# Kernel tuning notes

Hardware: AMD Instinct MI355X
Metric: run time of the kernel (lower is better)

Reference implementation:

```python
import jax, jax.numpy as jnp
import numpy as np

B = 32       # batch
IN_N = 32    # input capsules
IN_D = 16    # input capsule dim (== out_d)
H = 14       # input spatial
OUT_N = 32   # output capsules
OUT_D = 16
HO = 7       # parent grid h_out = w_out
HID = 64     # Linformer projection dim
EPS = 1e-5


def _gconv(x, w, groups):
    # x: [b, C, H, W], w: [C_out, C_in/groups, kh, kw]; stride 1, pad 1
    return jax.lax.conv_general_dilated(
        x, w, window_strides=(1, 1), padding=((1, 1), (1, 1)),
        dimension_numbers=("NCHW", "OIHW", "NCHW"), feature_group_count=groups)


def setup_inputs() -> dict:
    key = jax.random.key(0)
    ks = jax.random.split(key, 7)
    current_pose = jax.random.normal(ks[0], (B, IN_N, H, H, IN_D), dtype=jnp.float32)
    next_pose = jax.random.normal(ks[1], (B, OUT_N, HO, HO, OUT_D), dtype=jnp.float32)
    # grouped conv weights (torch layout OIHW, groups = IN_N)
    current_w = 0.05 * jax.random.normal(ks[2], (IN_N * IN_D, IN_D, 3, 3), dtype=jnp.float32)
    next_w = 0.05 * jax.random.normal(ks[3], (OUT_N * OUT_D, OUT_N * OUT_D // IN_N, 3, 3), dtype=jnp.float32)
    E_proj = 0.02 * jax.random.normal(ks[4], (IN_N, H * H, HID), dtype=jnp.float32)
    rel_embedd = jax.random.normal(ks[5], (IN_D, HO * HO), dtype=jnp.float32)
    ln_gamma = jnp.ones((OUT_D,), dtype=jnp.float32)
    ln_beta = jnp.zeros((OUT_D,), dtype=jnp.float32)
    return {
        "current_pose": current_pose, "next_pose": next_pose,
        "current_w": current_w, "next_w": next_w,
        "E_proj": E_proj, "rel_embedd": rel_embedd,
        "ln_gamma": ln_gamma, "ln_beta": ln_beta,
        "num_iter": 1,
    }


def reference(current_pose, next_pose, current_w, next_w, E_proj, rel_embedd,
              ln_gamma, ln_beta, num_iter):
    b = current_pose.shape[0]
    # 5D -> [b, n*d, H, W]
    cp = current_pose.transpose(0, 2, 3, 1, 4).reshape(b, H, H, IN_N * IN_D)
    cp = cp.transpose(0, 3, 1, 2)
    cp = _gconv(cp, current_w, IN_N)                       # [b, n*d, H, H]
    # headwise Linformer key projection
    cp = cp.reshape(b, IN_D, IN_N, 1, H * H)
    k = jnp.matmul(cp, E_proj)                             # [b, d, n, 1, HID]
    k = k.reshape(b, IN_D, IN_N * HID).transpose(0, 2, 1)  # [b, n*HID, d]
    rel = jnp.broadcast_to(rel_embedd.T[None], (b, HO * HO, IN_D))
    k = jnp.concatenate([k, rel], axis=1)                  # [b, N, d]

    # parent pose -> queries
    q = next_pose.transpose(0, 2, 3, 1, 4).reshape(b, HO, HO, OUT_N * OUT_D)
    q = q.transpose(0, 3, 1, 2)
    q = _gconv(q, next_w, IN_N)                            # [b, out_n*out_d, HO, HO]
    q = q.reshape(b, OUT_N * HO * HO, OUT_D)               # [b, J, d]

    dots = jnp.einsum("bje,bie->bji", q, k) * (IN_D ** -0.5)  # [b, J, N]
    dots = jax.nn.softmax(dots, axis=-2)                   # softmax over queries j
    out = jnp.einsum("bji,bie->bje", dots, k)              # [b, J, d]

    out = out.reshape(b, OUT_N * IN_D, HO, HO)
    out = _gconv(out, next_w, IN_N)
    out = out.reshape(b, OUT_N, HO, HO, IN_D)

    # LayerNorm over last dim (dropout rate = 0)
    mu = out.mean(-1, keepdims=True)
    var = ((out - mu) ** 2).mean(-1, keepdims=True)
    out = (out - mu) / jnp.sqrt(var + EPS) * ln_gamma + ln_beta
    return out
```

## Files before the change

kernel.cpp:

```cpp
#include <hip/hip_runtime.h>

typedef unsigned short u16;
typedef __attribute__((ext_vector_type(8))) short short8;
typedef __attribute__((ext_vector_type(4))) float floatx4;

#define MFMA16(a, b, c) __builtin_amdgcn_mfma_f32_16x16x32_bf16(a, b, c, 0, 0, 0)

__device__ inline u16 bf16rn(float x) {
    unsigned u = __float_as_uint(x);
    u += 0x7fffu + ((u >> 16) & 1u);
    return (u16)(u >> 16);
}
__device__ inline float bf16tof(u16 h) { return __uint_as_float(((unsigned)h) << 16); }
__device__ inline short8 ld8(const u16* p) { return *(const short8*)p; }

__global__ __launch_bounds__(256) void k_ecvt2(const float* __restrict__ E,
                                               const float* __restrict__ rel,
                                               const float* __restrict__ w,
                                               u16* __restrict__ EhT,
                                               u16* __restrict__ ElT,
                                               u16* __restrict__ Kh,
                                               u16* __restrict__ Kl,
                                               u16* __restrict__ KhT,
                                               u16* __restrict__ KlT,
                                               float* __restrict__ w2) {
    int blk = blockIdx.x, tid = threadIdx.x;
    if (blk < 32) {
        __shared__ float ep[196 * 65];
        int m = blk;
        const float* eb = E + (size_t)m * 12544;
        for (int t = tid; t < 12544; t += 256) {
            int p = t >> 6, h = t & 63;
            ep[p * 65 + h] = eb[t];
        }
        __syncthreads();
        for (int t = tid; t < 64 * 224; t += 256) {
            int h = t / 224, p = t % 224;
            float v = (p < 196) ? ep[p * 65 + h] : 0.f;
            u16 hi = bf16rn(v);
            u16 lo = bf16rn(v - bf16tof(hi));
            EhT[(size_t)m * 14336 + t] = hi;
            ElT[(size_t)m * 14336 + t] = lo;
        }
    } else if (blk < 64) {
        int b = blk - 32;
        size_t bK = (size_t)b * 2112;
        size_t bT = (size_t)b * 33792;
#pragma unroll
        for (int k = 0; k < 4; ++k) {
            int idx = tid + k * 256;
            int row = idx >> 4, e = idx & 15;
            int i = 2048 + row;
            float v = (row < 49) ? rel[e * 49 + row] : 0.f;
            u16 h = bf16rn(v);
            u16 l = bf16rn(v - bf16tof(h));
            Kh[(bK + i) * 16 + e] = h;
            Kl[(bK + i) * 16 + e] = l;
            KhT[bT + (size_t)e * 2112 + i] = h;
            KlT[bT + (size_t)e * 2112 + i] = l;
        }
    } else {
        int g0 = (blk - 64) * 4;
        for (int t = tid; t < 4 * 2304; t += 256) {
            int g = g0 + t / 2304, r = t % 2304;
            int oc = r / 144, rr = r % 144;
            w2[(size_t)g * 2304 + (rr / 9) * 144 + oc * 9 + (rr % 9)] =
                w[(size_t)g * 2304 + r];
        }
    }
}

__global__ __launch_bounds__(256) void k_conv14(const float* __restrict__ pose,
                                                const float* __restrict__ w2,
                                                float* __restrict__ out) {
    int blk = blockIdx.x;
    int oh = blk & 1, bg = blk >> 1;
    int tid = threadIdx.x;
    __shared__ float patch[16 * 256];
#pragma unroll
    for (int k = 0; k < 16; ++k) patch[k * 256 + tid] = 0.f;
    __syncthreads();
    const float* pin = pose + (size_t)bg * 3136;
    for (int t = tid; t < 3136; t += 256) {
        int p = t >> 4, ic = t & 15;
        int y = p / 14, x = p % 14;
        patch[ic * 256 + (y + 1) * 16 + (x + 1)] = pin[t];
    }
    __syncthreads();
    int g = bg & 31;
    const float* wg = w2 + (size_t)g * 2304 + oh * 72;
    float* po = out + (size_t)bg * 3136 + oh * 8 * 196;
    if (tid < 196) {
        int y = tid / 14, x = tid % 14;
        int base = (y + 1) * 16 + (x + 1);
        float acc[8];
#pragma unroll
        for (int oc = 0; oc < 8; ++oc) acc[oc] = 0.f;
        for (int ic = 0; ic < 16; ++ic) {
            const float* pr = patch + ic * 256 + base;
            float win[9];
#pragma unroll
            for (int ky = 0; ky < 3; ++ky)
#pragma unroll
                for (int kx = 0; kx < 3; ++kx)
                    win[ky * 3 + kx] = pr[(ky - 1) * 16 + (kx - 1)];
            const float* wi = wg + ic * 144;
#pragma unroll
            for (int oc = 0; oc < 8; ++oc)
#pragma unroll
                for (int kk = 0; kk < 9; ++kk)
                    acc[oc] += win[kk] * wi[oc * 9 + kk];
        }
#pragma unroll
        for (int oc = 0; oc < 8; ++oc) po[oc * 196 + tid] = acc[oc];
    }
}

__global__ __launch_bounds__(64) void k_conv7(const float* __restrict__ in,
                                              const float* __restrict__ in2,
                                              const float* __restrict__ w,
                                              float* __restrict__ out, int mode) {
    int blk = blockIdx.x;
    int oh = blk & 1, bg = blk >> 1;
    int tid = threadIdx.x;
    __shared__ float patch[16 * 144];
    for (int t = tid; t < 16 * 144; t += 64) patch[t] = 0.f;
    __syncthreads();
    const float* pin = in + (size_t)bg * 784;
    if (mode == 1) {
        for (int t = tid; t < 784; t += 64) {
            int p = t >> 4, ic = t & 15;
            int y = p / 7, x = p % 7;
            patch[ic * 144 + (y + 1) * 16 + (x + 1)] = pin[t];
        }
    } else {
        const float* pin2 = in2 + (size_t)bg * 784;
        for (int t = tid; t < 784; t += 64) {
            int ic = t / 49, p = t % 49;
            int y = p / 7, x = p % 7;
            patch[ic * 144 + (y + 1) * 16 + (x + 1)] = pin[t] + pin2[t];
        }
    }
    __syncthreads();
    int g = bg & 31;
    const float* wg = w + (size_t)g * 2304 + (size_t)oh * 8 * 144;
    float* po = out + (size_t)bg * 784 + (size_t)oh * 8 * 49;
    if (tid < 49) {
        int y = tid / 7, x = tid % 7;
        int base = (y + 1) * 16 + (x + 1);
        float acc[8];
#pragma unroll
        for (int oc = 0; oc < 8; ++oc) acc[oc] = 0.f;
        for (int ic = 0; ic < 16; ++ic) {
            const float* pr = patch + ic * 144 + base;
            float win[9];
#pragma unroll
            for (int ky = 0; ky < 3; ++ky)
#pragma unroll
                for (int kx = 0; kx < 3; ++kx)
                    win[ky * 3 + kx] = pr[(ky - 1) * 16 + (kx - 1)];
            const float* wi = wg + ic * 9;
#pragma unroll
            for (int oc = 0; oc < 8; ++oc)
#pragma unroll
                for (int kk = 0; kk < 9; ++kk)
                    acc[oc] += win[kk] * wi[oc * 144 + kk];
        }
#pragma unroll
        for (int oc = 0; oc < 8; ++oc) po[oc * 49 + tid] = acc[oc];
    }
}

__global__ __launch_bounds__(256) void k_kproj2(const float* __restrict__ cpconv,
                                                const u16* __restrict__ EhT,
                                                const u16* __restrict__ ElT,
                                                u16* __restrict__ Kh,
                                                u16* __restrict__ Kl,
                                                u16* __restrict__ KhT,
                                                u16* __restrict__ KlT) {
    int blk = blockIdx.x;
    int b = blk >> 5, m = blk & 31;
    int wave = threadIdx.x >> 6, lane = threadIdx.x & 63;
    int ht = wave;
    int n = lane & 15, quad = lane >> 4;

    const float* arow = cpconv + ((size_t)b * 512 + (size_t)n * 32 + m) * 196;
    const u16* bhrow = EhT + ((size_t)m * 64 + ht * 16 + n) * 224;
    const u16* blrow = ElT + ((size_t)m * 64 + ht * 16 + n) * 224;

    floatx4 c = {0.f, 0.f, 0.f, 0.f};
#pragma unroll
    for (int pc = 0; pc < 7; ++pc) {
        int p0 = pc * 32 + quad * 8;
        float av[8];
        if (p0 <= 188) {
            float4 x = *(const float4*)(arow + p0);
            float4 y = *(const float4*)(arow + p0 + 4);
            av[0]=x.x; av[1]=x.y; av[2]=x.z; av[3]=x.w;
            av[4]=y.x; av[5]=y.y; av[6]=y.z; av[7]=y.w;
        } else {
#pragma unroll
            for (int k2 = 0; k2 < 8; ++k2) av[k2] = (p0 + k2 < 196) ? arow[p0 + k2] : 0.f;
        }
        short8 ah, al;
#pragma unroll
        for (int k2 = 0; k2 < 8; ++k2) {
            u16 h = bf16rn(av[k2]);
            ah[k2] = (short)h;
            al[k2] = (short)bf16rn(av[k2] - bf16tof(h));
        }
        short8 bh = ld8(bhrow + pc * 32 + quad * 8);
        short8 bl = ld8(blrow + pc * 32 + quad * 8);
        c = MFMA16(ah, bh, c);
        c = MFMA16(ah, bl, c);
        c = MFMA16(al, bh, c);
    }
    int i = m * 64 + ht * 16 + n;
    size_t bK = (size_t)b * 2112;
    size_t bT = (size_t)b * 33792;
    u16 h[4], l[4];
#pragma unroll
    for (int r = 0; r < 4; ++r) {
        h[r] = bf16rn(c[r]);
        l[r] = bf16rn(c[r] - bf16tof(h[r]));
    }
    *(uint2*)(Kh + (bK + i) * 16 + quad * 4) =
        make_uint2((unsigned)h[0] | ((unsigned)h[1] << 16), (unsigned)h[2] | ((unsigned)h[3] << 16));
    *(uint2*)(Kl + (bK + i) * 16 + quad * 4) =
        make_uint2((unsigned)l[0] | ((unsigned)l[1] << 16), (unsigned)l[2] | ((unsigned)l[3] << 16));
#pragma unroll
    for (int r = 0; r < 4; ++r) {
        KhT[bT + (size_t)(quad * 4 + r) * 2112 + i] = h[r];
        KlT[bT + (size_t)(quad * 4 + r) * 2112 + i] = l[r];
    }
}

__global__ __launch_bounds__(256) void k_cvt(const float* __restrict__ qconv,
                                             u16* __restrict__ Qp) {
    int gid = blockIdx.x * 256 + threadIdx.x;
    const float4* q4 = (const float4*)(qconv + (size_t)gid * 16);
    float4 t0 = q4[0], t1 = q4[1], t2 = q4[2], t3 = q4[3];
    float v[16] = {t0.x,t0.y,t0.z,t0.w, t1.x,t1.y,t1.z,t1.w,
                   t2.x,t2.y,t2.z,t2.w, t3.x,t3.y,t3.z,t3.w};
    unsigned hw[8], lw[8];
#pragma unroll
    for (int t = 0; t < 8; ++t) {
        float x0 = v[2*t] * 0.25f, x1 = v[2*t+1] * 0.25f;
        u16 h0 = bf16rn(x0), h1 = bf16rn(x1);
        u16 l0 = bf16rn(x0 - bf16tof(h0)), l1 = bf16rn(x1 - bf16tof(h1));
        hw[t] = (unsigned)h0 | ((unsigned)h1 << 16);
        lw[t] = (unsigned)l0 | ((unsigned)l1 << 16);
    }
    uint4* r4 = (uint4*)(Qp + (size_t)gid * 32);
    r4[0] = make_uint4(hw[0], hw[1], hw[2], hw[3]);
    r4[1] = make_uint4(hw[4], hw[5], hw[6], hw[7]);
    r4[2] = make_uint4(lw[0], lw[1], lw[2], lw[3]);
    r4[3] = make_uint4(lw[4], lw[5], lw[6], lw[7]);
}

__global__ __launch_bounds__(256) void k_stats4(const u16* __restrict__ Qp,
                                                const u16* __restrict__ Kh,
                                                const u16* __restrict__ Kl,
                                                float* __restrict__ dpart) {
    int blk = blockIdx.x;
    int b = blk / 34; int rem = blk % 34; int jh = rem / 17; int tb = rem % 17;
    int wave = threadIdx.x >> 6, lane = threadIdx.x & 63;
    int it2 = tb * 4 + wave;
    if (it2 >= 66) return;
    int ibase = it2 * 32;
    int n = lane & 15, quad = lane >> 4;
    size_t bK = (size_t)b * 2112;
    const u16* kb = Kh + (bK + ibase + n) * 16 + (quad & 1) * 8;
    const u16* lb = Kl + (bK + ibase + n) * 16 + (quad & 1) * 8;
    short8 bh0 = ld8(kb), bh1 = ld8(kb + 256);
    short8 bl0 = ld8(lb), bl1 = ld8(lb + 256);
    const u16* qb = Qp + (size_t)b * 50176 + (size_t)jh * 49 * 512 + n * 32 + quad * 8;
    floatx4 d0 = {0.f,0.f,0.f,0.f}, d1 = {0.f,0.f,0.f,0.f};
    short8 a0 = ld8(qb), a1 = ld8(qb + 512);
    for (int c = 0; c < 49; ++c) {
        short8 a2 = (c + 2 < 49) ? ld8(qb + (size_t)(c + 2) * 512) : a0;
        floatx4 s0 = {0.f,0.f,0.f,0.f}, s1 = {0.f,0.f,0.f,0.f};
        s0 = MFMA16(a0, bh0, s0);
        s0 = MFMA16(a0, bl0, s0);
        s1 = MFMA16(a0, bh1, s1);
        s1 = MFMA16(a0, bl1, s1);
        d0.x += __expf(s0.x); d0.y += __expf(s0.y);
        d0.z += __expf(s0.z); d0.w += __expf(s0.w);
        d1.x += __expf(s1.x); d1.y += __expf(s1.y);
        d1.z += __expf(s1.z); d1.w += __expf(s1.w);
        a0 = a1; a1 = a2;
    }
    float t0 = d0.x + d0.y + d0.z + d0.w;
    float t1 = d1.x + d1.y + d1.z + d1.w;
    t0 += __shfl_xor(t0, 16); t0 += __shfl_xor(t0, 32);
    t1 += __shfl_xor(t1, 16); t1 += __shfl_xor(t1, 32);
    if (quad == 0) {
        dpart[(size_t)jh * 67584 + bK + ibase + n]      = t0;
        dpart[(size_t)jh * 67584 + bK + ibase + 16 + n] = t1;
    }
}

__global__ __launch_bounds__(256) void k_pv5(const u16* __restrict__ Qp,
                                             const u16* __restrict__ Kh,
                                             const u16* __restrict__ Kl,
                                             const u16* __restrict__ KhT,
                                             const u16* __restrict__ KlT,
                                             const float* __restrict__ dpart,
                                             float* __restrict__ opart) {
    __shared__ __align__(16) u16 sH[2][32][16];
    __shared__ __align__(16) u16 sL[2][32][16];
    __shared__ __align__(16) u16 tH[2][16][32];
    __shared__ __align__(16) u16 tL[2][16][32];
    __shared__ __align__(16) u16 w16[4][16][40];
    __shared__ float rll[2][32];

    int blk = blockIdx.x;
    int b = blk / 50; int rem = blk % 50; int jtb = rem >> 1; int ih = rem & 1;
    int tid = threadIdx.x, wave = tid >> 6, lane = tid & 63;
    int n = lane & 15, quad = lane >> 4, qh = quad & 1;
    int jt = jtb * 4 + wave;
    int jtc = jt < 98 ? jt : 97;
    int i0 = ih * 1056;
    size_t bK = (size_t)b * 2112;
    size_t bT = (size_t)b * 33792;
    const float* d0p = dpart + bK;
    const float* d1p = dpart + 67584 + bK;

    short8 aq = ld8(Qp + ((size_t)b * 1568 + (size_t)jtc * 16 + n) * 32 + quad * 8);

    int role = wave, L = lane;
    uint4 sreg; float dv = 1.f;
    auto ldchunk = [&](int c) {
        int i0c = i0 + c * 32;
        if (role == 0)      sreg = *(const uint4*)(Kh  + (bK + i0c + (L >> 1)) * 16 + (L & 1) * 8);
        else if (role == 1) sreg = *(const uint4*)(Kl  + (bK + i0c + (L >> 1)) * 16 + (L & 1) * 8);
        else if (role == 2) sreg = *(const uint4*)(KhT + bT + (size_t)(L >> 2) * 2112 + i0c + (L & 3) * 8);
        else {
            sreg = *(const uint4*)(KlT + bT + (size_t)(L >> 2) * 2112 + i0c + (L & 3) * 8);
            if (L < 32) dv = d0p[i0c + L] + d1p[i0c + L];
        }
    };
    auto stchunk = [&](int bf) {
        if (role == 0)      *(uint4*)(&sH[bf][L >> 1][(L & 1) * 8]) = sreg;
        else if (role == 1) *(uint4*)(&sL[bf][L >> 1][(L & 1) * 8]) = sreg;
        else if (role == 2) *(uint4*)(&tH[bf][L >> 2][(L & 3) * 8]) = sreg;
        else {
            *(uint4*)(&tL[bf][L >> 2][(L & 3) * 8]) = sreg;
            if (L < 32) rll[bf][L] = 1.0f / dv;
        }
    };

    floatx4 o = {0.f, 0.f, 0.f, 0.f};

    ldchunk(0); stchunk(0); ldchunk(1);
    __syncthreads();
    for (int c = 0; c < 33; ++c) {
        int cb = c & 1;
        short8 sh0 = ld8(&sH[cb][n][qh * 8]);
        short8 sh1 = ld8(&sH[cb][16 + n][qh * 8]);
        short8 sl0 = ld8(&sL[cb][n][qh * 8]);
        short8 sl1 = ld8(&sL[cb][16 + n][qh * 8]);
        short8 th  = ld8(&tH[cb][n][quad * 8]);
        short8 tl  = ld8(&tL[cb][n][quad * 8]);
        float r0 = rll[cb][n], r1 = rll[cb][16 + n];
        floatx4 s0 = {0.f,0.f,0.f,0.f};
        s0 = MFMA16(aq, sh0, s0);
        s0 = MFMA16(aq, sl0, s0);
        floatx4 s1 = {0.f,0.f,0.f,0.f};
        s1 = MFMA16(aq, sh1, s1);
        s1 = MFMA16(aq, sl1, s1);
#pragma unroll
        for (int r = 0; r < 4; ++r) {
            float w0 = __expf(s0[r]) * r0;
            float w1 = __expf(s1[r]) * r1;
            w16[wave][quad * 4 + r][n]      = (u16)(__float_as_uint(w0) >> 16);
            w16[wave][quad * 4 + r][16 + n] = (u16)(__float_as_uint(w1) >> 16);
        }
        asm volatile("s_waitcnt lgkmcnt(0)" ::: "memory");
        short8 aw = ld8(&w16[wave][n][quad * 8]);
        o = MFMA16(aw, th, o);
        o = MFMA16(aw, tl, o);
        if (c < 32) stchunk((c + 1) & 1);
        if (c < 31) ldchunk(c + 2);
        __syncthreads();
    }
    if (jt < 98) {
        float* ob = opart + (size_t)ih * 802816 + ((size_t)b * 1568 + (size_t)jt * 16) * 16;
#pragma unroll
        for (int r = 0; r < 4; ++r) ob[(quad * 4 + r) * 16 + n] = o[r];
    }
}

__global__ __launch_bounds__(256) void k_ln(const float* __restrict__ x,
                                            const float* __restrict__ gamma,
                                            const float* __restrict__ beta,
                                            float* __restrict__ out, int ngroups) {
    int g = blockIdx.x * 256 + threadIdx.x;
    if (g >= ngroups) return;
    const float4* xp = (const float4*)(x + (size_t)g * 16);
    float4 x0 = xp[0], x1 = xp[1], x2 = xp[2], x3 = xp[3];
    float sum = x0.x + x0.y + x0.z + x0.w + x1.x + x1.y + x1.z + x1.w
              + x2.x + x2.y + x2.z + x2.w + x3.x + x3.y + x3.z + x3.w;
    float mu = sum * 0.0625f;
    float var = 0.f;
    var += (x0.x-mu)*(x0.x-mu) + (x0.y-mu)*(x0.y-mu) + (x0.z-mu)*(x0.z-mu) + (x0.w-mu)*(x0.w-mu);
    var += (x1.x-mu)*(x1.x-mu) + (x1.y-mu)*(x1.y-mu) + (x1.z-mu)*(x1.z-mu) + (x1.w-mu)*(x1.w-mu);
    var += (x2.x-mu)*(x2.x-mu) + (x2.y-mu)*(x2.y-mu) + (x2.z-mu)*(x2.z-mu) + (x2.w-mu)*(x2.w-mu);
    var += (x3.x-mu)*(x3.x-mu) + (x3.y-mu)*(x3.y-mu) + (x3.z-mu)*(x3.z-mu) + (x3.w-mu)*(x3.w-mu);
    float rstd = rsqrtf(var * 0.0625f + 1e-5f);
    const float4* gp = (const float4*)gamma;
    const float4* bp = (const float4*)beta;
    float4 g0 = gp[0], g1 = gp[1], g2 = gp[2], g3 = gp[3];
    float4 be0 = bp[0], be1 = bp[1], be2 = bp[2], be3 = bp[3];
    float4 o0, o1, o2, o3;
    o0.x = (x0.x-mu)*rstd*g0.x + be0.x; o0.y = (x0.y-mu)*rstd*g0.y + be0.y;
    o0.z = (x0.z-mu)*rstd*g0.z + be0.z; o0.w = (x0.w-mu)*rstd*g0.w + be0.w;
    o1.x = (x1.x-mu)*rstd*g1.x + be1.x; o1.y = (x1.y-mu)*rstd*g1.y + be1.y;
    o1.z = (x1.z-mu)*rstd*g1.z + be1.z; o1.w = (x1.w-mu)*rstd*g1.w + be1.w;
    o2.x = (x2.x-mu)*rstd*g2.x + be2.x; o2.y = (x2.y-mu)*rstd*g2.y + be2.y;
    o2.z = (x2.z-mu)*rstd*g2.z + be2.z; o2.w = (x2.w-mu)*rstd*g2.w + be2.w;
    o3.x = (x3.x-mu)*rstd*g3.x + be3.x; o3.y = (x3.y-mu)*rstd*g3.y + be3.y;
    o3.z = (x3.z-mu)*rstd*g3.z + be3.z; o3.w = (x3.w-mu)*rstd*g3.w + be3.w;
    float4* op = (float4*)(out + (size_t)g * 16);
    op[0] = o0; op[1] = o1; op[2] = o2; op[3] = o3;
}

extern "C" void kernel_launch(void* const* d_in, const int* in_sizes, int n_in,
                              void* d_out, int out_size, void* d_ws, size_t ws_size,
                              hipStream_t stream) {
    const float* current_pose = (const float*)d_in[0];
    const float* next_pose    = (const float*)d_in[1];
    const float* current_w    = (const float*)d_in[2];
    const float* next_w       = (const float*)d_in[3];
    const float* E_proj       = (const float*)d_in[4];
    const float* rel          = (const float*)d_in[5];
    const float* ln_gamma     = (const float*)d_in[6];
    const float* ln_beta      = (const float*)d_in[7];
    float* out = (float*)d_out;
    float* ws  = (float*)d_ws;

    float* cpconv = ws;
    float* conv2  = ws;
    float* opart  = ws + 802816;
    float* dpart  = ws + 2408448;
    float* qconv  = ws + 3211264;
    float* w2     = ws + 4014080;
    u16*   ub     = (u16*)(ws + 4087808);
    u16* Qp  = ub;
    u16* Kh  = ub + 1605632;
    u16* Kl  = ub + 2686976;
    u16* KhT = ub + 3768320;
    u16* KlT = ub + 4849664;
    u16* EhT = ub + 5931008;
    u16* ElT = ub + 6389760;

    k_ecvt2 <<<72,   256, 0, stream>>>(E_proj, rel, current_w, EhT, ElT,
                                       Kh, Kl, KhT, KlT, w2);
    k_conv14<<<2048, 256, 0, stream>>>(current_pose, w2, cpconv);
    k_conv7 <<<2048, 64,  0, stream>>>(next_pose, next_pose, next_w, qconv, 1);
    k_cvt   <<<196,  256, 0, stream>>>(qconv, Qp);
    k_kproj2<<<1024, 256, 0, stream>>>(cpconv, EhT, ElT, Kh, Kl, KhT, KlT);
    k_stats4<<<1088, 256, 0, stream>>>(Qp, Kh, Kl, dpart);
    k_pv5   <<<1600, 256, 0, stream>>>(Qp, Kh, Kl, KhT, KlT, dpart, opart);
    k_conv7 <<<2048, 64,  0, stream>>>(opart, opart + 802816, next_w, conv2, 0);
    k_ln    <<<196,  256, 0, stream>>>(conv2, ln_gamma, ln_beta, out, 50176);
}
```

Measured before the change: 230.0 us.

## Prescale V by softmax denominators and keep P in registers via permlane swaps

Adds a small kernel that folds the per-key softmax reciprocal into the transposed K values (stored as hi/lo bf16 split), removing the per-chunk reciprocal and multiply from the PV kernel. The PV kernel now computes S transposed so the exp'd probabilities can be packed and rearranged with permlane32/16 swaps directly into MFMA A operands, eliminating the LDS round-trip and wait. Each wave also handles two query tiles, reusing loaded K/V chunks and halving the grid. It costs an extra kernel launch and read/write pass over V, and changes rounding of the scaled V and of P (truncation packing).

Result: no change. 231.0 us (+0.4%).

```diff
diff --git a/kernel.cpp b/kernel.cpp
--- a/kernel.cpp
+++ b/kernel.cpp
@@ -3,6 +3,7 @@
 typedef unsigned short u16;
 typedef __attribute__((ext_vector_type(8))) short short8;
 typedef __attribute__((ext_vector_type(4))) float floatx4;
+typedef __attribute__((ext_vector_type(4))) unsigned uintx4;
 
 #define MFMA16(a, b, c) __builtin_amdgcn_mfma_f32_16x16x32_bf16(a, b, c, 0, 0, 0)
 
@@ -13,6 +14,9 @@
 }
 __device__ inline float bf16tof(u16 h) { return __uint_as_float(((unsigned)h) << 16); }
 __device__ inline short8 ld8(const u16* p) { return *(const short8*)p; }
+__device__ inline unsigned pack2(float a, float b) {
+    return __builtin_amdgcn_perm(__float_as_uint(b), __float_as_uint(a), 0x07060302u);
+}
 
 __global__ __launch_bounds__(256) void k_ecvt2(const float* __restrict__ E,
                                                const float* __restrict__ rel,
@@ -300,57 +304,78 @@
     }
 }
 
-__global__ __launch_bounds__(256) void k_pv5(const u16* __restrict__ Qp,
+__global__ __launch_bounds__(256) void k_vscale(const float* __restrict__ dpart,
+                                                u16* __restrict__ VhT,
+                                                u16* __restrict__ VlT) {
+    int gid = blockIdx.x * 256 + threadIdx.x;
+    int ic = gid % 264;
+    int be = gid / 264;
+    int b = be >> 4, e = be & 15;
+    size_t off = (size_t)b * 33792 + (size_t)e * 2112 + (size_t)ic * 8;
+    short8 h8 = ld8(VhT + off);
+    short8 l8 = ld8(VlT + off);
+    const float* dp = dpart + (size_t)b * 2112 + ic * 8;
+    float4 da0 = *(const float4*)dp;
+    float4 da1 = *(const float4*)(dp + 4);
+    float4 db0 = *(const float4*)(dp + 67584);
+    float4 db1 = *(const float4*)(dp + 67588);
+    float d[8] = {da0.x+db0.x, da0.y+db0.y, da0.z+db0.z, da0.w+db0.w,
+                  da1.x+db1.x, da1.y+db1.y, da1.z+db1.z, da1.w+db1.w};
+    short8 oh, ol;
+#pragma unroll
+    for (int k = 0; k < 8; ++k) {
+        float v = bf16tof((u16)h8[k]) + bf16tof((u16)l8[k]);
+        float sv = v / d[k];
+        u16 hh = bf16rn(sv);
+        ol[k] = (short)bf16rn(sv - bf16tof(hh));
+        oh[k] = (short)hh;
+    }
+    *(short8*)(VhT + off) = oh;
+    *(short8*)(VlT + off) = ol;
+}
+
+__global__ __launch_bounds__(256) void k_pv6(const u16* __restrict__ Qp,
                                              const u16* __restrict__ Kh,
                                              const u16* __restrict__ Kl,
-                                             const u16* __restrict__ KhT,
-                                             const u16* __restrict__ KlT,
-                                             const float* __restrict__ dpart,
+                                             const u16* __restrict__ VhT,
+                                             const u16* __restrict__ VlT,
                                              float* __restrict__ opart) {
     __shared__ __align__(16) u16 sH[2][32][16];
     __shared__ __align__(16) u16 sL[2][32][16];
     __shared__ __align__(16) u16 tH[2][16][32];
     __shared__ __align__(16) u16 tL[2][16][32];
-    __shared__ __align__(16) u16 w16[4][16][40];
-    __shared__ float rll[2][32];
 
     int blk = blockIdx.x;
-    int b = blk / 50; int rem = blk % 50; int jtb = rem >> 1; int ih = rem & 1;
+    int b = blk / 26; int rem = blk % 26; int jtb = rem >> 1; int ih = rem & 1;
     int tid = threadIdx.x, wave = tid >> 6, lane = tid & 63;
     int n = lane & 15, quad = lane >> 4, qh = quad & 1;
-    int jt = jtb * 4 + wave;
-    int jtc = jt < 98 ? jt : 97;
+    int jt0 = (jtb * 4 + wave) * 2;
+    int jc0 = jt0     < 98 ? jt0     : 97;
+    int jc1 = jt0 + 1 < 98 ? jt0 + 1 : 97;
     int i0 = ih * 1056;
     size_t bK = (size_t)b * 2112;
     size_t bT = (size_t)b * 33792;
-    const float* d0p = dpart + bK;
-    const float* d1p = dpart + 67584 + bK;
-
-    short8 aq = ld8(Qp + ((size_t)b * 1568 + (size_t)jtc * 16 + n) * 32 + quad * 8);
+
+    short8 aq0 = ld8(Qp + ((size_t)b * 1568 + (size_t)jc0 * 16 + n) * 32 + quad * 8);
+    short8 aq1 = ld8(Qp + ((size_t)b * 1568 + (size_t)jc1 * 16 + n) * 32 + quad * 8);
 
     int role = wave, L = lane;
-    uint4 sreg; float dv = 1.f;
+    uint4 sreg;
     auto ldchunk = [&](int c) {
         int i0c = i0 + c * 32;
         if (role == 0)      sreg = *(const uint4*)(Kh  + (bK + i0c + (L >> 1)) * 16 + (L & 1) * 8);
         else if (role == 1) sreg = *(const uint4*)(Kl  + (bK + i0c + (L >> 1)) * 16 + (L & 1) * 8);
-        else if (role == 2) sreg = *(const uint4*)(KhT + bT + (size_t)(L >> 2) * 2112 + i0c + (L & 3) * 8);
-        else {
-            sreg = *(const uint4*)(KlT + bT + (size_t)(L >> 2) * 2112 + i0c + (L & 3) * 8);
-            if (L < 32) dv = d0p[i0c + L] + d1p[i0c + L];
-        }
+        else if (role == 2) sreg = *(const uint4*)(VhT + bT + (size_t)(L >> 2) * 2112 + i0c + (L & 3) * 8);
+        else                sreg = *(const uint4*)(VlT + bT + (size_t)(L >> 2) * 2112 + i0c + (L & 3) * 8);
     };
     auto stchunk = [&](int bf) {
         if (role == 0)      *(uint4*)(&sH[bf][L >> 1][(L & 1) * 8]) = sreg;
         else if (role == 1) *(uint4*)(&sL[bf][L >> 1][(L & 1) * 8]) = sreg;
         else if (role == 2) *(uint4*)(&tH[bf][L >> 2][(L & 3) * 8]) = sreg;
-        else {
-            *(uint4*)(&tL[bf][L >> 2][(L & 3) * 8]) = sreg;
-            if (L < 32) rll[bf][L] = 1.0f / dv;
-        }
+        else                *(uint4*)(&tL[bf][L >> 2][(L & 3) * 8]) = sreg;
     };
 
-    floatx4 o = {0.f, 0.f, 0.f, 0.f};
+    floatx4 o0 = {0.f, 0.f, 0.f, 0.f}, o1 = {0.f, 0.f, 0.f, 0.f};
 
     ldchunk(0); stchunk(0); ldchunk(1);
     __syncthreads();
@@ -362,32 +387,58 @@
         short8 sl1 = ld8(&sL[cb][16 + n][qh * 8]);
         short8 th  = ld8(&tH[cb][n][quad * 8]);
         short8 tl  = ld8(&tL[cb][n][quad * 8]);
-        float r0 = rll[cb][n], r1 = rll[cb][16 + n];
-        floatx4 s0 = {0.f,0.f,0.f,0.f};
-        s0 = MFMA16(aq, sh0, s0);
-        s0 = MFMA16(aq, sl0, s0);
-        floatx4 s1 = {0.f,0.f,0.f,0.f};
-        s1 = MFMA16(aq, sh1, s1);
-        s1 = MFMA16(aq, sl1, s1);
-#pragma unroll
-        for (int r = 0; r < 4; ++r) {
-            float w0 = __expf(s0[r]) * r0;
-            float w1 = __expf(s1[r]) * r1;
-            w16[wave][quad * 4 + r][n]      = (u16)(__float_as_uint(w0) >> 16);
-            w16[wave][quad * 4 + r][16 + n] = (u16)(__float_as_uint(w1) >> 16);
-        }
-        asm volatile("s_waitcnt lgkmcnt(0)" ::: "memory");
-        short8 aw = ld8(&w16[wave][n][quad * 8]);
-        o = MFMA16(aw, th, o);
-        o = MFMA16(aw, tl, o);
+
+        {
+            floatx4 s0 = {0.f,0.f,0.f,0.f}, s1 = {0.f,0.f,0.f,0.f};
+            s0 = MFMA16(sh0, aq0, s0);
+            s0 = MFMA16(sl0, aq0, s0);
+            s1 = MFMA16(sh1, aq0, s1);
+            s1 = MFMA16(sl1, aq0, s1);
+            unsigned u00 = pack2(__expf(s0[0]), __expf(s0[1]));
+            unsigned u01 = pack2(__expf(s0[2]), __expf(s0[3]));
+            unsigned u10 = pack2(__expf(s1[0]), __expf(s1[1]));
+            unsigned u11 = pack2(__expf(s1[2]), __expf(s1[3]));
+            asm("v_permlane32_swap_b32 %0, %1" : "+v"(u00), "+v"(u10));
+            asm("v_permlane32_swap_b32 %0, %1" : "+v"(u01), "+v"(u11));
+            asm("v_permlane16_swap_b32 %0, %1" : "+v"(u00), "+v"(u10));
+            asm("v_permlane16_swap_b32 %0, %1" : "+v"(u01), "+v"(u11));
+            uintx4 uv = {u00, u01, u10, u11};
+            short8 aw = __builtin_bit_cast(short8, uv);
+            o0 = MFMA16(aw, th, o0);
+            o0 = MFMA16(aw, tl, o0);
+        }
+        {
+            floatx4 s0 = {0.f,0.f,0.f,0.f}, s1 = {0.f,0.f,0.f,0.f};
+            s0 = MFMA16(sh0, aq1, s0);
+            s0 = MFMA16(sl0, aq1, s0);
+            s1 = MFMA16(sh1, aq1, s1);
+            s1 = MFMA16(sl1, aq1, s1);
+            unsigned u00 = pack2(__expf(s0[0]), __expf(s0[1]));
+            unsigned u01 = pack2(__expf(s0[2]), __expf(s0[3]));
+            unsigned u10 = pack2(__expf(s1[0]), __expf(s1[1]));
+            unsigned u11 = pack2(__expf(s1[2]), __expf(s1[3]));
+            asm("v_permlane32_swap_b32 %0, %1" : "+v"(u00), "+v"(u10));
+            asm("v_permlane32_swap_b32 %0, %1" : "+v"(u01), "+v"(u11));
+            asm("v_permlane16_swap_b32 %0, %1" : "+v"(u00), "+v"(u10));
+            asm("v_permlane16_swap_b32 %0, %1" : "+v"(u01), "+v"(u11));
+            uintx4 uv = {u00, u01, u10, u11};
+            short8 aw = __builtin_bit_cast(short8, uv);
+            o1 = MFMA16(aw, th, o1);
+            o1 = MFMA16(aw, tl, o1);
+        }
         if (c < 32) stchunk((c + 1) & 1);
         if (c < 31) ldchunk(c + 2);
         __syncthreads();
     }
-    if (jt < 98) {
-        float* ob = opart + (size_t)ih * 802816 + ((size_t)b * 1568 + (size_t)jt * 16) * 16;
-#pragma unroll
-        for (int r = 0; r < 4; ++r) ob[(quad * 4 + r) * 16 + n] = o[r];
+    if (jt0 < 98) {
+        float* ob = opart + (size_t)ih * 802816 + ((size_t)b * 1568 + (size_t)jt0 * 16) * 16;
+#pragma unroll
+        for (int r = 0; r < 4; ++r) ob[(quad * 4 + r) * 16 + n] = o0[r];
+    }
+    if (jt0 + 1 < 98) {
+        float* ob = opart + (size_t)ih * 802816 + ((size_t)b * 1568 + (size_t)(jt0 + 1) * 16) * 16;
+#pragma unroll
+        for (int r = 0; r < 4; ++r) ob[(quad * 4 + r) * 16 + n] = o1[r];
     }
 }
 
@@ -461,7 +512,8 @@
     k_cvt   <<<196,  256, 0, stream>>>(qconv, Qp);
     k_kproj2<<<1024, 256, 0, stream>>>(cpconv, EhT, ElT, Kh, Kl, KhT, KlT);
     k_stats4<<<1088, 256, 0, stream>>>(Qp, Kh, Kl, dpart);
-    k_pv5   <<<1600, 256, 0, stream>>>(Qp, Kh, Kl, KhT, KlT, dpart, opart);
+    k_vscale<<<528,  256, 0, stream>>>(dpart, KhT, KlT);
+    k_pv6   <<<832,  256, 0, stream>>>(Qp, Kh, Kl, KhT, KlT, opart);
     k_conv7 <<<2048, 64,  0, stream>>>(opart, opart + 802816, next_w, conv2, 0);
     k_ln    <<<196,  256, 0, stream>>>(conv2, ln_gamma, ln_beta, out, 50176);
 }
```
